# Kernel optimization log

Measured on AMD Instinct MI355X. Metric: run time of the kernel, lower is better.

Reference implementation:

```python
import jax, jax.numpy as jnp
import numpy as np

N_BOOK = 16  # == len_code; C() loop is only consistent when len_code == n_book


def setup_inputs() -> dict:
    key = jax.random.key(0)
    k1, k2 = jax.random.split(key)
    N = 32768
    D = 256        # len_code * n_book = 16 * 16
    n_classes = 4096
    features = jax.random.normal(k1, (N, D), dtype=jnp.float32)
    # Prototypes passed transposed relative to storage: [len_code*n_book, n_classes]
    Prototypes = jax.random.normal(k2, (D, n_classes), dtype=jnp.float32)
    return {"features": features, "Prototypes": Prototypes}


def reference(features, Prototypes):
    # Faithful to GPQSoftMaxNet.C: per-book matmul, concat over books, mean.
    # features: [N, len_code*n_book] split along dim 1 into chunks of width n_book
    # Prototypes: [len_code*n_book, n_classes] split along dim 0 into chunks of height n_book
    n_book = N_BOOK
    N, D = features.shape
    n_classes = Prototypes.shape[1]
    f = features.reshape(N, -1, n_book)          # [N, n_book(=len_code), n_book]
    P = Prototypes.reshape(-1, n_book, n_classes)  # [n_book(=len_code), n_book, n_classes]
    # mean over books of per-book GEMMs, fused into one einsum (no [N,C,n_book] intermediate)
    logits = jnp.einsum('nbd,bdc->nc', f, P) / jnp.float32(n_book)
    return logits
```

## Files before the change

kernel.cpp:

```cpp
#include <hip/hip_runtime.h>
#include <hip/hip_bf16.h>

typedef __attribute__((ext_vector_type(8))) short short8;
typedef __attribute__((ext_vector_type(4))) float f32x4;

static constexpr int MT = 32768;
static constexpr int KT = 256;
static constexpr int CT = 4096;

__device__ __forceinline__ unsigned short f2b(float f) {
  unsigned int b = __float_as_uint(f);
  b += 0x7FFFu + ((b >> 16) & 1u);
  return (unsigned short)(b >> 16);
}

__global__ void __launch_bounds__(256) cvt_kernel(const float* __restrict__ A,
                                                  const float* __restrict__ B,
                                                  unsigned short* __restrict__ Abf,
                                                  unsigned short* __restrict__ Bt) {
  __shared__ unsigned short tile[32][33];
  int bid = blockIdx.x, tid = threadIdx.x;
  if (bid < 4096) {
    int i = bid * 256 + tid;
    const float4 v0 = reinterpret_cast<const float4*>(A)[2 * i];
    const float4 v1 = reinterpret_cast<const float4*>(A)[2 * i + 1];
    short8 o;
    o[0] = (short)f2b(v0.x); o[1] = (short)f2b(v0.y);
    o[2] = (short)f2b(v0.z); o[3] = (short)f2b(v0.w);
    o[4] = (short)f2b(v1.x); o[5] = (short)f2b(v1.y);
    o[6] = (short)f2b(v1.z); o[7] = (short)f2b(v1.w);
    reinterpret_cast<short8*>(Abf)[i] = o;
  } else {
    int b = bid - 4096;
    int c0 = (b & 127) * 32, k0 = (b >> 7) * 32;
    int tx = tid & 31, ty0 = tid >> 5;
#pragma unroll
    for (int i = 0; i < 4; ++i) {
      int ty = ty0 + i * 8;
      tile[ty][tx] = f2b(B[(size_t)(k0 + ty) * CT + c0 + tx]);
    }
    __syncthreads();
#pragma unroll
    for (int i = 0; i < 4; ++i) {
      int cy = ty0 + i * 8;
      Bt[(size_t)(c0 + cy) * KT + k0 + tx] = tile[tx][cy];
    }
  }
}

__device__ __forceinline__ void gload16(const void* g, void* l) {
  __builtin_amdgcn_global_load_lds(
      (const __attribute__((address_space(1))) void*)g,
      (__attribute__((address_space(3))) void*)l, 16, 0, 0);
}

__global__ void __launch_bounds__(512, 4) gemm_kernel(const unsigned short* __restrict__ Abf,
                                                      const unsigned short* __restrict__ Btw,
                                                      float* __restrict__ O) {
  constexpr int BK = 64;
  __shared__ __align__(16) char smem[48 * 1024];
  unsigned short* Al = (unsigned short*)smem;
  unsigned short* Bl = (unsigned short*)(smem + 16384);
  float* eb = (float*)smem;

  int bid = blockIdx.x;
  int wg = (bid & 7) * 512 + (bid >> 3);
  int tc = wg & 15;
  int tr = wg >> 4;
  int r0 = tr * 128, c0 = tc * 256;

  int tid = threadIdx.x;
  int lane = tid & 63, wid = tid >> 6;
  int wr = wid >> 2, wc = wid & 3;
  int l15 = lane & 15, l4 = lane >> 4;

  f32x4 acc[4][4] = {};

  for (int t = 0; t < KT / BK; ++t) {
    if (t) __syncthreads();
#pragma unroll
    for (int i = 0; i < 2; ++i) {
      int c = i * 512 + wid * 64 + lane;
      int sc = (c & 7) ^ ((c >> 3) & 7);
      gload16(Abf + (size_t)(r0 + (c >> 3)) * KT + t * BK + sc * 8,
              Al + (i * 512 + wid * 64) * 8);
    }
#pragma unroll
    for (int i = 0; i < 4; ++i) {
      int c = i * 512 + wid * 64 + lane;
      int sc = (c & 7) ^ ((c >> 3) & 7);
      gload16(Btw + (size_t)(c0 + (c >> 3)) * KT + t * BK + sc * 8,
              Bl + (i * 512 + wid * 64) * 8);
    }
    __syncthreads();

#pragma unroll
    for (int ks = 0; ks < 2; ++ks) {
      short8 af[4], bf[4];
#pragma unroll
      for (int m = 0; m < 4; ++m) {
        int row = wr * 64 + m * 16 + l15;
        int slot = (ks * 4 + l4) ^ (l15 & 7);
        af[m] = *reinterpret_cast<const short8*>(Al + row * BK + slot * 8);
      }
#pragma unroll
      for (int n = 0; n < 4; ++n) {
        int row = wc * 64 + n * 16 + l15;
        int slot = (ks * 4 + l4) ^ (l15 & 7);
        bf[n] = *reinterpret_cast<const short8*>(Bl + row * BK + slot * 8);
      }
#pragma unroll
      for (int n = 0; n < 4; ++n)
#pragma unroll
        for (int m = 0; m < 4; ++m)
          acc[n][m] = __builtin_amdgcn_mfma_f32_16x16x32_bf16(bf[n], af[m], acc[n][m], 0, 0, 0);
    }
  }

  const float s = 1.0f / 16.0f;
#pragma unroll
  for (int p = 0; p < 4; ++p) {
    __syncthreads();
    if (wr == (p >> 1)) {
#pragma unroll
      for (int mm = 0; mm < 2; ++mm) {
        int m = (p & 1) * 2 + mm;
#pragma unroll
        for (int n = 0; n < 4; ++n) {
          f32x4 v = acc[n][m];
          v[0] *= s; v[1] *= s; v[2] *= s; v[3] *= s;
          *reinterpret_cast<f32x4*>(
              &eb[(mm * 16 + l15) * 264 + wc * 64 + n * 16 + l4 * 4]) = v;
        }
      }
    }
    __syncthreads();
#pragma unroll
    for (int i = 0; i < 4; ++i) {
      int r = i * 8 + wid;
      f32x4 v = *reinterpret_cast<const f32x4*>(&eb[r * 264 + lane * 4]);
      __builtin_nontemporal_store(v, reinterpret_cast<f32x4*>(
          O + (size_t)(r0 + p * 32 + r) * CT + c0 + lane * 4));
    }
  }
}

__global__ void __launch_bounds__(256) naive_kernel(const float* __restrict__ A,
                                                    const float* __restrict__ B,
                                                    float* __restrict__ O) {
  size_t i = (size_t)blockIdx.x * 256 + threadIdx.x;
  int col = (int)(i & (size_t)(CT - 1));
  int row = (int)(i >> 12);
  float s = 0.f;
  for (int k = 0; k < KT; ++k)
    s += A[(size_t)row * KT + k] * B[(size_t)k * CT + col];
  O[i] = s * (1.0f / 16.0f);
}

extern "C" void kernel_launch(void* const* d_in, const int* in_sizes, int n_in,
                              void* d_out, int out_size, void* d_ws, size_t ws_size,
                              hipStream_t stream) {
  const float* A = (const float*)d_in[0];
  const float* B = (const float*)d_in[1];
  float* O = (float*)d_out;
  const size_t needA = (size_t)MT * KT * sizeof(unsigned short);
  const size_t needB = (size_t)CT * KT * sizeof(unsigned short);
  if (ws_size >= needA + needB) {
    unsigned short* Abf = (unsigned short*)d_ws;
    unsigned short* Btw = (unsigned short*)((char*)d_ws + needA);
    cvt_kernel<<<4096 + 1024, 256, 0, stream>>>(A, B, Abf, Btw);
    gemm_kernel<<<(MT / 128) * (CT / 256), 512, 0, stream>>>(Abf, Btw, O);
  } else {
    naive_kernel<<<(unsigned)((size_t)MT * CT / 256), 256, 0, stream>>>(A, B, O);
  }
}
```

Measured before the change: 121.3 us.

## Fuse A fp32-to-bf16 conversion into GEMM tile loads

Removes the separate pass that converts features to bf16 in the workspace. The GEMM now loads fp32 A tiles straight into registers, rounds them to bf16, and writes them swizzled into LDS. Only the prototype transpose-convert kernel is kept. This avoids writing and re-reading a 16 MB bf16 copy of A, but A is now read as fp32 once per column tile (16 times), and the A loads become synchronous register loads instead of direct global-to-LDS loads.

```diff
diff --git a/kernel.cpp b/kernel.cpp
--- a/kernel.cpp
+++ b/kernel.cpp
@@ -14,37 +14,22 @@
   return (unsigned short)(b >> 16);
 }
 
-__global__ void __launch_bounds__(256) cvt_kernel(const float* __restrict__ A,
-                                                  const float* __restrict__ B,
-                                                  unsigned short* __restrict__ Abf,
-                                                  unsigned short* __restrict__ Bt) {
+__global__ void __launch_bounds__(256) cvtB_kernel(const float* __restrict__ B,
+                                                   unsigned short* __restrict__ Bt) {
   __shared__ unsigned short tile[32][33];
-  int bid = blockIdx.x, tid = threadIdx.x;
-  if (bid < 4096) {
-    int i = bid * 256 + tid;
-    const float4 v0 = reinterpret_cast<const float4*>(A)[2 * i];
-    const float4 v1 = reinterpret_cast<const float4*>(A)[2 * i + 1];
-    short8 o;
-    o[0] = (short)f2b(v0.x); o[1] = (short)f2b(v0.y);
-    o[2] = (short)f2b(v0.z); o[3] = (short)f2b(v0.w);
-    o[4] = (short)f2b(v1.x); o[5] = (short)f2b(v1.y);
-    o[6] = (short)f2b(v1.z); o[7] = (short)f2b(v1.w);
-    reinterpret_cast<short8*>(Abf)[i] = o;
-  } else {
-    int b = bid - 4096;
-    int c0 = (b & 127) * 32, k0 = (b >> 7) * 32;
-    int tx = tid & 31, ty0 = tid >> 5;
+  int b = blockIdx.x, tid = threadIdx.x;
+  int c0 = (b & 127) * 32, k0 = (b >> 7) * 32;
+  int tx = tid & 31, ty0 = tid >> 5;
 #pragma unroll
-    for (int i = 0; i < 4; ++i) {
-      int ty = ty0 + i * 8;
-      tile[ty][tx] = f2b(B[(size_t)(k0 + ty) * CT + c0 + tx]);
-    }
-    __syncthreads();
+  for (int i = 0; i < 4; ++i) {
+    int ty = ty0 + i * 8;
+    tile[ty][tx] = f2b(B[(size_t)(k0 + ty) * CT + c0 + tx]);
+  }
+  __syncthreads();
 #pragma unroll
-    for (int i = 0; i < 4; ++i) {
-      int cy = ty0 + i * 8;
-      Bt[(size_t)(c0 + cy) * KT + k0 + tx] = tile[tx][cy];
-    }
+  for (int i = 0; i < 4; ++i) {
+    int cy = ty0 + i * 8;
+    Bt[(size_t)(c0 + cy) * KT + k0 + tx] = tile[tx][cy];
   }
 }
 
@@ -54,7 +39,7 @@
       (__attribute__((address_space(3))) void*)l, 16, 0, 0);
 }
 
-__global__ void __launch_bounds__(512, 4) gemm_kernel(const unsigned short* __restrict__ Abf,
+__global__ void __launch_bounds__(512, 4) gemm_kernel(const float* __restrict__ A,
                                                       const unsigned short* __restrict__ Btw,
                                                       float* __restrict__ O) {
   constexpr int BK = 64;
@@ -78,19 +63,32 @@
 
   for (int t = 0; t < KT / BK; ++t) {
     if (t) __syncthreads();
+    f32x4 alo[2], ahi[2];
 #pragma unroll
     for (int i = 0; i < 2; ++i) {
-      int c = i * 512 + wid * 64 + lane;
-      int sc = (c & 7) ^ ((c >> 3) & 7);
-      gload16(Abf + (size_t)(r0 + (c >> 3)) * KT + t * BK + sc * 8,
-              Al + (i * 512 + wid * 64) * 8);
+      int c = i * 512 + tid;
+      const float* src = A + (size_t)(r0 + (c >> 3)) * KT + t * BK + (c & 7) * 8;
+      alo[i] = *reinterpret_cast<const f32x4*>(src);
+      ahi[i] = *reinterpret_cast<const f32x4*>(src + 4);
     }
 #pragma unroll
     for (int i = 0; i < 4; ++i) {
-      int c = i * 512 + wid * 64 + lane;
+      int c = i * 512 + tid;
       int sc = (c & 7) ^ ((c >> 3) & 7);
       gload16(Btw + (size_t)(c0 + (c >> 3)) * KT + t * BK + sc * 8,
-              Bl + (i * 512 + wid * 64) * 8);
+              Bl + (i * 512 + (tid & ~63)) * 8);
+    }
+#pragma unroll
+    for (int i = 0; i < 2; ++i) {
+      int c = i * 512 + tid;
+      int row = c >> 3, slot = (c & 7) ^ (row & 7);
+      short8 o;
+#pragma unroll
+      for (int j = 0; j < 4; ++j) {
+        o[j] = (short)f2b(alo[i][j]);
+        o[4 + j] = (short)f2b(ahi[i][j]);
+      }
+      *reinterpret_cast<short8*>(Al + row * BK + slot * 8) = o;
     }
     __syncthreads();
 
@@ -163,13 +161,11 @@
   const float* A = (const float*)d_in[0];
   const float* B = (const float*)d_in[1];
   float* O = (float*)d_out;
-  const size_t needA = (size_t)MT * KT * sizeof(unsigned short);
   const size_t needB = (size_t)CT * KT * sizeof(unsigned short);
-  if (ws_size >= needA + needB) {
-    unsigned short* Abf = (unsigned short*)d_ws;
-    unsigned short* Btw = (unsigned short*)((char*)d_ws + needA);
-    cvt_kernel<<<4096 + 1024, 256, 0, stream>>>(A, B, Abf, Btw);
-    gemm_kernel<<<(MT / 128) * (CT / 256), 512, 0, stream>>>(Abf, Btw, O);
+  if (ws_size >= needB) {
+    unsigned short* Btw = (unsigned short*)d_ws;
+    cvtB_kernel<<<1024, 256, 0, stream>>>(B, Btw);
+    gemm_kernel<<<(MT / 128) * (CT / 256), 512, 0, stream>>>(A, Btw, O);
   } else {
     naive_kernel<<<(unsigned)((size_t)MT * CT / 256), 256, 0, stream>>>(A, B, O);
   }
```

Result: slower. 125.6 us (+3.6%).

## Double-buffer GEMM K-tiles with BK=32 to overlap global loads with MFMA

Applied to the files above, without the earlier changes.

Halves the K-tile to 32 and splits LDS into two buffers, so the direct-to-LDS global load of the next tile is issued before computing on the current one. A partial vmcnt wait and raw s_barrier replace the full syncthreads. The swizzle is rewritten to suit the narrower 4-slot rows. The goal is to hide global load latency behind MFMA work, at the cost of more barriers per K step and a hand-counted vmcnt that must match the number of outstanding loads.

```diff
diff --git a/kernel.cpp b/kernel.cpp
--- a/kernel.cpp
+++ b/kernel.cpp
@@ -57,10 +57,10 @@
 __global__ void __launch_bounds__(512, 4) gemm_kernel(const unsigned short* __restrict__ Abf,
                                                       const unsigned short* __restrict__ Btw,
                                                       float* __restrict__ O) {
-  constexpr int BK = 64;
+  constexpr int BK = 32, NT_ = KT / BK;
   __shared__ __align__(16) char smem[48 * 1024];
-  unsigned short* Al = (unsigned short*)smem;
-  unsigned short* Bl = (unsigned short*)(smem + 16384);
+  unsigned short* Albuf[2] = {(unsigned short*)smem, (unsigned short*)(smem + 8192)};
+  unsigned short* Blbuf[2] = {(unsigned short*)(smem + 16384), (unsigned short*)(smem + 32768)};
   float* eb = (float*)smem;
 
   int bid = blockIdx.x;
@@ -73,48 +73,52 @@
   int lane = tid & 63, wid = tid >> 6;
   int wr = wid >> 2, wc = wid & 3;
   int l15 = lane & 15, l4 = lane >> 4;
+  const int sw = l4 ^ ((l15 >> 1) & 3);
 
   f32x4 acc[4][4] = {};
 
-  for (int t = 0; t < KT / BK; ++t) {
-    if (t) __syncthreads();
+  auto stage = [&](int buf, int t) {
+    {
+      int c = tid;
+      int sc = (c & 3) ^ ((c >> 3) & 3);
+      gload16(Abf + (size_t)(r0 + (c >> 2)) * KT + t * BK + sc * 8,
+              Albuf[buf] + (wid * 64) * 8);
+    }
 #pragma unroll
     for (int i = 0; i < 2; ++i) {
-      int c = i * 512 + wid * 64 + lane;
-      int sc = (c & 7) ^ ((c >> 3) & 7);
-      gload16(Abf + (size_t)(r0 + (c >> 3)) * KT + t * BK + sc * 8,
-              Al + (i * 512 + wid * 64) * 8);
+      int c = i * 512 + tid;
+      int sc = (c & 3) ^ ((c >> 3) & 3);
+      gload16(Btw + (size_t)(c0 + (c >> 2)) * KT + t * BK + sc * 8,
+              Blbuf[buf] + (i * 512 + wid * 64) * 8);
     }
+  };
+
+  stage(0, 0);
 #pragma unroll
-    for (int i = 0; i < 4; ++i) {
-      int c = i * 512 + wid * 64 + lane;
-      int sc = (c & 7) ^ ((c >> 3) & 7);
-      gload16(Btw + (size_t)(c0 + (c >> 3)) * KT + t * BK + sc * 8,
-              Bl + (i * 512 + wid * 64) * 8);
-    }
-    __syncthreads();
+  for (int t = 0; t < NT_; ++t) {
+    const int cur = t & 1;
+    if (t + 1 < NT_) stage(cur ^ 1, t + 1);
+    if (t + 1 < NT_) asm volatile("s_waitcnt vmcnt(3)" ::: "memory");
+    else             asm volatile("s_waitcnt vmcnt(0)" ::: "memory");
+    __builtin_amdgcn_s_barrier();
 
+    short8 af[4], bf[4];
 #pragma unroll
-    for (int ks = 0; ks < 2; ++ks) {
-      short8 af[4], bf[4];
+    for (int m = 0; m < 4; ++m)
+      af[m] = *reinterpret_cast<const short8*>(
+          Albuf[cur] + (wr * 64 + m * 16 + l15) * BK + sw * 8);
 #pragma unroll
-      for (int m = 0; m < 4; ++m) {
-        int row = wr * 64 + m * 16 + l15;
-        int slot = (ks * 4 + l4) ^ (l15 & 7);
-        af[m] = *reinterpret_cast<const short8*>(Al + row * BK + slot * 8);
-      }
+    for (int n = 0; n < 4; ++n)
+      bf[n] = *reinterpret_cast<const short8*>(
+          Blbuf[cur] + (wc * 64 + n * 16 + l15) * BK + sw * 8);
 #pragma unroll
-      for (int n = 0; n < 4; ++n) {
-        int row = wc * 64 + n * 16 + l15;
-        int slot = (ks * 4 + l4) ^ (l15 & 7);
-        bf[n] = *reinterpret_cast<const short8*>(Bl + row * BK + slot * 8);
-      }
+    for (int n = 0; n < 4; ++n)
 #pragma unroll
-      for (int n = 0; n < 4; ++n)
-#pragma unroll
-        for (int m = 0; m < 4; ++m)
-          acc[n][m] = __builtin_amdgcn_mfma_f32_16x16x32_bf16(bf[n], af[m], acc[n][m], 0, 0, 0);
-    }
+      for (int m = 0; m < 4; ++m)
+        acc[n][m] = __builtin_amdgcn_mfma_f32_16x16x32_bf16(bf[n], af[m], acc[n][m], 0, 0, 0);
+
+    asm volatile("s_waitcnt lgkmcnt(0)" ::: "memory");
+    __builtin_amdgcn_s_barrier();
   }
 
   const float s = 1.0f / 16.0f;
```

New measurement: 119.1 us (median of 2 runs). Within noise of the previous version (-1.7%).
